# Kernel optimization log

Hardware: AMD Instinct MI355X
Metric: run time of the kernel (lower is better)

## Reference

```python
import jax, jax.numpy as jnp
import numpy as np

N_NODES = 50000
N_EDGES = 400000
IN_DIM = 64
HID = 128
HEADS = 4
NEG_SLOPE = 0.2


def gat_conv(x, src, dst, W, a_src, a_dst, b, heads, out_ch, concat):
    N = x.shape[0]
    h = (x @ W).reshape(N, heads, out_ch)                 # [N,H,C]
    alpha_s = jnp.einsum('nhc,hc->nh', h, a_src)          # [N,H]
    alpha_d = jnp.einsum('nhc,hc->nh', h, a_dst)
    e = jax.nn.leaky_relu(alpha_s[src] + alpha_d[dst], NEG_SLOPE)  # [E,H]
    m = jax.ops.segment_max(e, dst, num_segments=N)
    m = jnp.where(jnp.isfinite(m), m, 0.0)
    ex = jnp.exp(e - m[dst])
    s = jax.ops.segment_sum(ex, dst, num_segments=N)
    alpha = ex / s[dst]                                   # segment softmax over incoming edges
    out = jax.ops.segment_sum(h[src] * alpha[:, :, None], dst, num_segments=N)  # [N,H,C]
    out = out.reshape(N, heads * out_ch) if concat else out.mean(axis=1)
    return out + b


def setup_inputs() -> dict:
    key = jax.random.key(0)
    ks = jax.random.split(key, 20)
    g = lambda i, shape, sc: (jax.random.normal(ks[i], shape, jnp.float32) * sc)
    x = g(0, (N_NODES, IN_DIM), 1.0)
    edge_index = jax.random.randint(ks[1], (2, N_EDGES), 0, N_NODES, dtype=jnp.int32)
    d = {
        'x': x, 'edge_index': edge_index,
        'W1': g(2, (IN_DIM, HEADS * HID), 0.1), 'a_src1': g(3, (HEADS, HID), 0.1), 'a_dst1': g(4, (HEADS, HID), 0.1), 'b1': jnp.zeros((HEADS * HID,), jnp.float32),
        'W2': g(5, (HEADS * HID, HEADS * HID), 0.05), 'a_src2': g(6, (HEADS, HID), 0.1), 'a_dst2': g(7, (HEADS, HID), 0.1), 'b2': jnp.zeros((HEADS * HID,), jnp.float32),
        'W3': g(8, (HEADS * HID, HID), 0.05), 'a_src3': g(9, (1, HID), 0.1), 'a_dst3': g(10, (1, HID), 0.1), 'b3': jnp.zeros((HID,), jnp.float32),
        'fc1_w': g(11, (HID, HID // 2), 0.1), 'fc1_b': jnp.zeros((HID // 2,), jnp.float32),
        'fc2_w': g(12, (HID // 2, 1), 0.1), 'fc2_b': jnp.zeros((1,), jnp.float32),
    }
    return d


def reference(x, edge_index, W1, a_src1, a_dst1, b1, W2, a_src2, a_dst2, b2, W3, a_src3, a_dst3, b3, fc1_w, fc1_b, fc2_w, fc2_b):
    N = x.shape[0]
    loop = jnp.arange(N, dtype=edge_index.dtype)
    src = jnp.concatenate([edge_index[0], loop])  # PyG GATConv adds self-loops by default
    dst = jnp.concatenate([edge_index[1], loop])
    h = jax.nn.elu(gat_conv(x, src, dst, W1, a_src1, a_dst1, b1, HEADS, HID, True))
    h = jax.nn.elu(gat_conv(h, src, dst, W2, a_src2, a_dst2, b2, HEADS, HID, True))
    h = jax.nn.elu(gat_conv(h, src, dst, W3, a_src3, a_dst3, b3, 1, HID, False))
    h = jax.nn.relu(h @ fc1_w + fc1_b)
    return jax.nn.sigmoid(h @ fc2_w + fc2_b)  # [N, 1]
```

## Files before the change

kernel.cpp:

```cpp
#include <hip/hip_runtime.h>
#include <math.h>

typedef __attribute__((ext_vector_type(8))) short short8;
typedef __attribute__((ext_vector_type(4))) float f32x4;
typedef unsigned short u16;
typedef unsigned int u32;

__device__ inline u16 f2b(float f) {
  u32 u = __float_as_uint(f);
  return (u16)((u + 0x7FFFu + ((u >> 16) & 1u)) >> 16);
}
__device__ inline float b2f(u16 b) { return __uint_as_float((u32)b << 16); }
__device__ inline float lrelu(float v) { return v > 0.f ? v : 0.2f * v; }

__device__ inline void gld_lds16(const void* g, void* l) {
  __builtin_amdgcn_global_load_lds((const __attribute__((address_space(1))) void*)g,
                                   (__attribute__((address_space(3))) void*)l, 16, 0, 0);
}

__global__ void fused_prep(const float* __restrict__ x, u16* __restrict__ xb, int NX,
                           const float* __restrict__ W1, u16* __restrict__ Wt1,
                           const float* __restrict__ W2, u16* __restrict__ Wt2,
                           const float* __restrict__ W3, u16* __restrict__ Wt3,
                           const int* __restrict__ ei, int E0, int ET,
                           int* __restrict__ deg) {
  int i = blockIdx.x * blockDim.x + threadIdx.x;
  if (i < NX) {
    xb[i] = f2b(x[i]);
    return;
  }
  i -= NX;
  if (i < 64 * 512) {
    int k = i / 512, n = i % 512;
    Wt1[n * 64 + k] = f2b(W1[i]);
    return;
  }
  i -= 64 * 512;
  if (i < 512 * 512) {
    int k = i / 512, n = i % 512;
    Wt2[n * 512 + k] = f2b(W2[i]);
    return;
  }
  i -= 512 * 512;
  if (i < 512 * 128) {
    int k = i / 128, n = i % 128;
    Wt3[n * 512 + k] = f2b(W3[i]);
    return;
  }
  i -= 512 * 128;
  if (i < ET) {
    int d = (i < E0) ? ei[E0 + i] : (i - E0);
    atomicAdd(&deg[d], 1);
  }
}

__global__ __launch_bounds__(256) void gemm_bf16_gat(
    const u16* __restrict__ A, const u16* __restrict__ Bt, u16* __restrict__ Hb,
    const float* __restrict__ a_src, const float* __restrict__ a_dst,
    float* __restrict__ aS, float* __restrict__ aD, int M, int HC, int K, int Hh,
    int gy, int nStrips) {
  int mIdx, nIdx;
  if (nStrips == 4) {
    int l = blockIdx.x;
    int xcd = l & 7, k = l >> 3;
    nIdx = k & 3;
    mIdx = xcd + 8 * (k >> 2);
    if (mIdx >= gy) return;
  } else {
    mIdx = blockIdx.x;
    nIdx = 0;
  }
  __shared__ u16 As[128 * 32];
  __shared__ u16 Bs[128 * 32];
  __shared__ float sRed[2][2][128];
  const int tid = threadIdx.x;
  const int w = tid >> 6, lane = tid & 63;
  const int wm = w >> 1, wn = w & 1;
  const int q = lane >> 4, l15 = lane & 15;
  const int nBase = nIdx * 128;
  const int mBase = mIdx * 128;
  const int h = nBase >> 7;
  const int srow = lane >> 2;
  const int skc = (lane & 3) * 8;

  f32x4 acc[4][4];
#pragma unroll
  for (int i = 0; i < 4; ++i)
#pragma unroll
    for (int j = 0; j < 4; ++j) acc[i][j] = (f32x4){0.f, 0.f, 0.f, 0.f};

  for (int k0 = 0; k0 < K; k0 += 32) {
#pragma unroll
    for (int r = 0; r < 2; ++r) {
      int lrow = w * 32 + r * 16 + srow;
      int ga = mBase + lrow;
      if (ga >= M) ga = M - 1;
      gld_lds16(A + (size_t)ga * K + k0 + skc, &As[(w * 32 + r * 16) * 32]);
      int gb = nBase + lrow;
      gld_lds16(Bt + (size_t)gb * K + k0 + skc, &Bs[(w * 32 + r * 16) * 32]);
    }
    __syncthreads();
    short8 af[4], bf[4];
#pragma unroll
    for (int i = 0; i < 4; ++i)
      af[i] = *(const short8*)&As[(wm * 64 + i * 16 + l15) * 32 + q * 8];
#pragma unroll
    for (int j = 0; j < 4; ++j)
      bf[j] = *(const short8*)&Bs[(wn * 64 + j * 16 + l15) * 32 + q * 8];
#pragma unroll
    for (int i = 0; i < 4; ++i)
#pragma unroll
      for (int j = 0; j < 4; ++j)
        acc[i][j] = __builtin_amdgcn_mfma_f32_16x16x32_bf16(af[i], bf[j], acc[i][j], 0, 0, 0);
    __syncthreads();
  }

  float asv[4], adv[4];
#pragma unroll
  for (int j = 0; j < 4; ++j) {
    int cw = wn * 64 + j * 16 + l15;
    asv[j] = a_src[h * 128 + cw];
    adv[j] = a_dst[h * 128 + cw];
  }
#pragma unroll
  for (int mi = 0; mi < 4; ++mi) {
#pragma unroll
    for (int r = 0; r < 4; ++r) {
      int row = mBase + wm * 64 + mi * 16 + q * 4 + r;
      float s = 0.f, d = 0.f;
#pragma unroll
      for (int j = 0; j < 4; ++j) {
        float v = acc[mi][j][r];
        s = fmaf(v, asv[j], s);
        d = fmaf(v, adv[j], d);
        if (row < M) Hb[(size_t)row * HC + nBase + wn * 64 + j * 16 + l15] = f2b(v);
      }
#pragma unroll
      for (int o = 8; o; o >>= 1) {
        s += __shfl_xor(s, o);
        d += __shfl_xor(d, o);
      }
      if (l15 == 0) {
        int lr = wm * 64 + mi * 16 + q * 4 + r;
        sRed[0][wn][lr] = s;
        sRed[1][wn][lr] = d;
      }
    }
  }
  __syncthreads();
  if (tid < 128) {
    int row = mBase + tid;
    if (row < M) {
      aS[(size_t)row * Hh + h] = sRed[0][0][tid] + sRed[0][1][tid];
      aD[(size_t)row * Hh + h] = sRed[1][0][tid] + sRed[1][1][tid];
    }
  }
}

__global__ __launch_bounds__(256) void scan_chunk(const int* __restrict__ deg,
                                                  int* __restrict__ incl,
                                                  int* __restrict__ bsums, int N) {
  __shared__ int sdata[256];
  const int t = threadIdx.x;
  const int base = blockIdx.x * 2048;
  int v[8];
  int sum = 0;
#pragma unroll
  for (int i = 0; i < 8; ++i) {
    int idx = base + t * 8 + i;
    v[i] = (idx < N) ? deg[idx] : 0;
    sum += v[i];
  }
  sdata[t] = sum;
  __syncthreads();
  for (int off = 1; off < 256; off <<= 1) {
    int x = (t >= off) ? sdata[t - off] : 0;
    __syncthreads();
    sdata[t] += x;
    __syncthreads();
  }
  int run = (t > 0) ? sdata[t - 1] : 0;
#pragma unroll
  for (int i = 0; i < 8; ++i) {
    int idx = base + t * 8 + i;
    run += v[i];
    if (idx < N) incl[idx] = run;
  }
  if (t == 255) bsums[blockIdx.x] = sdata[255];
}

__global__ void scan_final(const int* __restrict__ incl, const int* __restrict__ bsums,
                           int* __restrict__ rowptr, int N, int nb) {
  int i = blockIdx.x * blockDim.x + threadIdx.x;
  if (i >= N) return;
  int chunk = i >> 11;
  int pre = 0;
  for (int j = 0; j < chunk; ++j) pre += bsums[j];
  rowptr[i + 1] = incl[i] + pre;
  if (i == 0) rowptr[0] = 0;
}

__global__ void csr_fill(const int* __restrict__ ei, int E0, int ET,
                         const int* __restrict__ rowptr, int* __restrict__ cnt,
                         int* __restrict__ csr_src) {
  int e = blockIdx.x * blockDim.x + threadIdx.x;
  if (e >= ET) return;
  int s, d;
  if (e < E0) { s = ei[e]; d = ei[E0 + e]; }
  else        { s = e - E0; d = e - E0; }
  int pos = atomicAdd(&cnt[d], 1);
  csr_src[rowptr[d] + pos] = s;
}

#define ACC8(pv, wgt)                                                  \
  acc[0] = fmaf(wgt, __uint_as_float(pv.x << 16), acc[0]);             \
  acc[1] = fmaf(wgt, __uint_as_float(pv.x & 0xffff0000u), acc[1]);     \
  acc[2] = fmaf(wgt, __uint_as_float(pv.y << 16), acc[2]);             \
  acc[3] = fmaf(wgt, __uint_as_float(pv.y & 0xffff0000u), acc[3]);     \
  acc[4] = fmaf(wgt, __uint_as_float(pv.z << 16), acc[4]);             \
  acc[5] = fmaf(wgt, __uint_as_float(pv.z & 0xffff0000u), acc[5]);     \
  acc[6] = fmaf(wgt, __uint_as_float(pv.w << 16), acc[6]);             \
  acc[7] = fmaf(wgt, __uint_as_float(pv.w & 0xffff0000u), acc[7]);

__global__ __launch_bounds__(256) void gat_fused_agg(
    const int* __restrict__ rowptr, const int* __restrict__ csr_src,
    const u16* __restrict__ Hb, const float* __restrict__ aSb,
    const float* __restrict__ aDb, const float* __restrict__ bias,
    u16* __restrict__ outB, float* __restrict__ outF, int N) {
  const int wid = (int)((blockIdx.x * (blockDim.x >> 6)) + (threadIdx.x >> 6));
  const int lane = threadIdx.x & 63;
  if (wid >= N) return;
  const int beg = rowptr[wid];
  const int deg = rowptr[wid + 1] - beg;

  const int h = lane >> 4;
  const int e16 = lane & 15;
  const int c0 = lane * 8;
  const int hbase = lane & 48;
  const float adh = aDb[(size_t)wid * 4 + h];
  float acc[8] = {};

  if (deg <= 16) {
    int srcv = 0;
    if (e16 < deg) srcv = csr_src[beg + e16];
    float av = aSb[(size_t)srcv * 4 + h];
    uint4 pC[4];
#pragma unroll
    for (int j = 0; j < 4; ++j)
      if (j < deg) {
        int s = __shfl(srcv, j);
        pC[j] = *(const uint4*)&Hb[(size_t)s * 512 + c0];
      }
    float l = (e16 < deg) ? lrelu(av + adh) : -1e30f;
    float m = l;
#pragma unroll
    for (int o = 8; o; o >>= 1) m = fmaxf(m, __shfl_xor(m, o));
    float pexp = (e16 < deg) ? __expf(l - m) : 0.f;
    float cs = pexp;
#pragma unroll
    for (int o = 8; o; o >>= 1) cs += __shfl_xor(cs, o);
    pexp *= (1.f / cs);
    int e = 0;
    for (; e + 4 < deg; e += 4) {
      uint4 pN[4];
      int rem = deg - e - 4;
#pragma unroll
      for (int j = 0; j < 4; ++j)
        if (j < rem) {
          int s = __shfl(srcv, e + 4 + j);
          pN[j] = *(const uint4*)&Hb[(size_t)s * 512 + c0];
        }
#pragma unroll
      for (int j = 0; j < 4; ++j) {
        float wgt = __shfl(pexp, hbase | (e + j));
        ACC8(pC[j], wgt)
      }
#pragma unroll
      for (int j = 0; j < 4; ++j) pC[j] = pN[j];
    }
#pragma unroll
    for (int j = 0; j < 4; ++j)
      if (j < deg - e) {
        float wgt = __shfl(pexp, hbase | (e + j));
        ACC8(pC[j], wgt)
      }
  } else {
    float m = -1e30f, ssum = 0.f;
    for (int c = 0; c < deg; c += 16) {
      const int ce = min(16, deg - c);
      int srcv = 0;
      float l = -1e30f;
      if (e16 < ce) {
        srcv = csr_src[beg + c + e16];
        l = lrelu(aSb[(size_t)srcv * 4 + h] + adh);
      }
      float cm = l;
#pragma unroll
      for (int o = 8; o; o >>= 1) cm = fmaxf(cm, __shfl_xor(cm, o));
      float pexp, cs;
      if (c == 0) {
        m = cm;
        pexp = __expf(l - m);
        cs = pexp;
#pragma unroll
        for (int o = 8; o; o >>= 1) cs += __shfl_xor(cs, o);
        ssum = cs;
      } else {
        float newm = fmaxf(m, cm);
        float r = __expf(m - newm);
        m = newm;
        pexp = __expf(l - m);
        cs = pexp;
#pragma unroll
        for (int o = 8; o; o >>= 1) cs += __shfl_xor(cs, o);
        ssum = ssum * r + cs;
#pragma unroll
        for (int i = 0; i < 8; ++i) acc[i] *= r;
      }
      int e = 0;
      for (; e + 4 <= ce; e += 4) {
        int se0 = __shfl(srcv, e + 0), se1 = __shfl(srcv, e + 1);
        int se2 = __shfl(srcv, e + 2), se3 = __shfl(srcv, e + 3);
        float w0 = __shfl(pexp, hbase | (e + 0)), w1 = __shfl(pexp, hbase | (e + 1));
        float w2 = __shfl(pexp, hbase | (e + 2)), w3 = __shfl(pexp, hbase | (e + 3));
        uint4 p0 = *(const uint4*)&Hb[(size_t)se0 * 512 + c0];
        uint4 p1 = *(const uint4*)&Hb[(size_t)se1 * 512 + c0];
        uint4 p2 = *(const uint4*)&Hb[(size_t)se2 * 512 + c0];
        uint4 p3 = *(const uint4*)&Hb[(size_t)se3 * 512 + c0];
        ACC8(p0, w0)
        ACC8(p1, w1)
        ACC8(p2, w2)
        ACC8(p3, w3)
      }
      for (; e < ce; ++e) {
        int se = __shfl(srcv, e);
        float wgt = __shfl(pexp, hbase | e);
        uint4 pv = *(const uint4*)&Hb[(size_t)se * 512 + c0];
        ACC8(pv, wgt)
      }
    }
    const float inv = 1.f / ssum;
#pragma unroll
    for (int i = 0; i < 8; ++i) acc[i] *= inv;
  }

  float bv[8];
  *(float4*)&bv[0] = *(const float4*)&bias[c0];
  *(float4*)&bv[4] = *(const float4*)&bias[c0 + 4];
  u16 packed[8];
#pragma unroll
  for (int i = 0; i < 8; ++i) {
    float v = acc[i] + bv[i];
    v = v > 0.f ? v : expm1f(v);
    acc[i] = v;
    packed[i] = f2b(v);
  }
  if (outB) *(uint4*)&outB[(size_t)wid * 512 + c0] = *(const uint4*)packed;
  if (outF) {
    *(float4*)&outF[(size_t)wid * 512 + c0] = make_float4(acc[0], acc[1], acc[2], acc[3]);
    *(float4*)&outF[(size_t)wid * 512 + c0 + 4] =
        make_float4(acc[4], acc[5], acc[6], acc[7]);
  }
}

__global__ __launch_bounds__(256) void gat_agg_h1(
    const int* __restrict__ rowptr, const int* __restrict__ csr_src,
    const u16* __restrict__ Hb, const float* __restrict__ aSb,
    const float* __restrict__ aDb, const float* __restrict__ bias,
    float* __restrict__ outF, int N) {
  const int wid = (int)((blockIdx.x * (blockDim.x >> 6)) + (threadIdx.x >> 6));
  const int lane = threadIdx.x & 63;
  if (wid >= N) return;
  const int beg = rowptr[wid];
  const int deg = rowptr[wid + 1] - beg;
  const int g = lane & 15;
  const int es = lane >> 4;
  const int c0 = g * 8;
  const float adh = aDb[wid];
  float acc[8] = {};

  if (deg <= 64) {
    int srcv = 0;
    if (lane < deg) srcv = csr_src[beg + lane];
    float av = aSb[srcv];
    const int dm1 = deg - 1;
    uint4 pC;
    {
      int s = __shfl(srcv, min(es, dm1));
      pC = *(const uint4*)&Hb[(size_t)s * 128 + c0];
    }
    float l = (lane < deg) ? lrelu(av + adh) : -1e30f;
    float m = l;
#pragma unroll
    for (int o = 32; o; o >>= 1) m = fmaxf(m, __shfl_xor(m, o));
    float pexp = (lane < deg) ? __expf(l - m) : 0.f;
    float cs = pexp;
#pragma unroll
    for (int o = 32; o; o >>= 1) cs += __shfl_xor(cs, o);
    pexp *= (1.f / cs);
    int t = 0;
    for (; t + 4 < deg; t += 4) {
      uint4 pN;
      {
        int s = __shfl(srcv, min(t + 4 + es, dm1));
        pN = *(const uint4*)&Hb[(size_t)s * 128 + c0];
      }
      float w = __shfl(pexp, t + es);
      ACC8(pC, w)
      pC = pN;
    }
    {
      int idx = t + es;
      float w = __shfl(pexp, min(idx, dm1));
      if (idx > dm1) w = 0.f;
      ACC8(pC, w)
    }
  } else {
    float m = -1e30f, ssum = 0.f;
    for (int c = 0; c < deg; c += 64) {
      const int ce = min(64, deg - c);
      int srcv = 0;
      float l = -1e30f;
      if (lane < ce) {
        srcv = csr_src[beg + c + lane];
        l = lrelu(aSb[srcv] + adh);
      }
      float cm = l;
#pragma unroll
      for (int o = 32; o; o >>= 1) cm = fmaxf(cm, __shfl_xor(cm, o));
      float pexp, cs;
      if (c == 0) {
        m = cm;
        pexp = __expf(l - m);
        cs = pexp;
#pragma unroll
        for (int o = 32; o; o >>= 1) cs += __shfl_xor(cs, o);
        ssum = cs;
      } else {
        float newm = fmaxf(m, cm);
        float r = __expf(m - newm);
        m = newm;
        pexp = __expf(l - m);
        cs = pexp;
#pragma unroll
        for (int o = 32; o; o >>= 1) cs += __shfl_xor(cs, o);
        ssum = ssum * r + cs;
#pragma unroll
        for (int i = 0; i < 8; ++i) acc[i] *= r;
      }
      for (int t = 0; t < ce; t += 4) {
        int idx = t + es;
        int se = __shfl(srcv, idx & 63);
        float wgt = __shfl(pexp, idx & 63);
        if (idx < ce) {
          uint4 pv = *(const uint4*)&Hb[(size_t)se * 128 + c0];
          ACC8(pv, wgt)
        }
      }
    }
    const float inv = 1.f / ssum;
#pragma unroll
    for (int i = 0; i < 8; ++i) acc[i] *= inv;
  }
#pragma unroll
  for (int i = 0; i < 8; ++i) {
    acc[i] += __shfl_xor(acc[i], 16);
    acc[i] += __shfl_xor(acc[i], 32);
  }
  if (lane < 16) {
    float o[8];
#pragma unroll
    for (int i = 0; i < 8; ++i) {
      float v = acc[i] + bias[c0 + i];
      o[i] = v > 0.f ? v : expm1f(v);
    }
    *(float4*)&outF[(size_t)wid * 128 + c0] = make_float4(o[0], o[1], o[2], o[3]);
    *(float4*)&outF[(size_t)wid * 128 + c0 + 4] = make_float4(o[4], o[5], o[6], o[7]);
  }
}

__global__ __launch_bounds__(256) void fc_head(const float* __restrict__ A,
                                               const float* __restrict__ B,
                                               const float* __restrict__ bias,
                                               const float* __restrict__ w2,
                                               const float* __restrict__ b2,
                                               float* __restrict__ out, int M) {
  __shared__ float As[16][64];
  __shared__ float Bs[16][64];
  __shared__ float sP[64][17];
  const int tid = threadIdx.x;
  const int tx = tid & 15, ty = tid >> 4;
  const int mBase = blockIdx.y * 64;
  const int aRow = tid >> 2;
  const int aK = (tid & 3) << 2;
  const int bC = tid & 63;
  const int bR0 = tid >> 6;
  const int K = 128, N = 64;
  float acc[4][4] = {};
  for (int k0 = 0; k0 < K; k0 += 16) {
    float4 av = make_float4(0.f, 0.f, 0.f, 0.f);
    int gr = mBase + aRow;
    if (gr < M) av = *(const float4*)&A[(size_t)gr * K + k0 + aK];
    As[aK + 0][aRow] = av.x;
    As[aK + 1][aRow] = av.y;
    As[aK + 2][aRow] = av.z;
    As[aK + 3][aRow] = av.w;
#pragma unroll
    for (int i = 0; i < 4; ++i) {
      int r = bR0 + i * 4;
      Bs[r][bC] = B[(size_t)(k0 + r) * N + bC];
    }
    __syncthreads();
#pragma unroll
    for (int k = 0; k < 16; ++k) {
      float4 a = *(const float4*)&As[k][ty * 4];
      float4 b = *(const float4*)&Bs[k][tx * 4];
      float ar[4] = {a.x, a.y, a.z, a.w};
      float br[4] = {b.x, b.y, b.z, b.w};
#pragma unroll
      for (int i = 0; i < 4; ++i)
#pragma unroll
        for (int j = 0; j < 4; ++j) acc[i][j] = fmaf(ar[i], br[j], acc[i][j]);
    }
    __syncthreads();
  }
  float4 bv = *(const float4*)&bias[tx * 4];
  float4 wv = *(const float4*)&w2[tx * 4];
#pragma unroll
  for (int i = 0; i < 4; ++i) {
    float p = 0.f;
    p = fmaf(fmaxf(acc[i][0] + bv.x, 0.f), wv.x, p);
    p = fmaf(fmaxf(acc[i][1] + bv.y, 0.f), wv.y, p);
    p = fmaf(fmaxf(acc[i][2] + bv.z, 0.f), wv.z, p);
    p = fmaf(fmaxf(acc[i][3] + bv.w, 0.f), wv.w, p);
    sP[ty * 4 + i][tx] = p;
  }
  __syncthreads();
  if (tid < 64) {
    int row = mBase + tid;
    if (row < M) {
      float s = 0.f;
#pragma unroll
      for (int t = 0; t < 16; ++t) s += sP[tid][t];
      out[row] = 1.f / (1.f + expf(-(s + b2[0])));
    }
  }
}

extern "C" void kernel_launch(void* const* d_in, const int* in_sizes, int n_in,
                              void* d_out, int out_size, void* d_ws, size_t ws_size,
                              hipStream_t stream) {
  const float* x    = (const float*)d_in[0];
  const int*   ei   = (const int*)d_in[1];
  const float* W1   = (const float*)d_in[2];
  const float* as1  = (const float*)d_in[3];
  const float* ad1  = (const float*)d_in[4];
  const float* b1   = (const float*)d_in[5];
  const float* W2   = (const float*)d_in[6];
  const float* as2  = (const float*)d_in[7];
  const float* ad2  = (const float*)d_in[8];
  const float* b2   = (const float*)d_in[9];
  const float* W3   = (const float*)d_in[10];
  const float* as3  = (const float*)d_in[11];
  const float* ad3  = (const float*)d_in[12];
  const float* b3   = (const float*)d_in[13];
  const float* fc1w = (const float*)d_in[14];
  const float* fc1b = (const float*)d_in[15];
  const float* fc2w = (const float*)d_in[16];
  const float* fc2b = (const float*)d_in[17];
  float* out = (float*)d_out;

  const int N  = in_sizes[0] / 64;
  const int E0 = in_sizes[1] / 2;
  const int ET = E0 + N;

  char* ws = (char*)d_ws;
  size_t off = 0;
  auto alloc = [&](size_t bytes) -> void* {
    void* p = ws + off;
    off += (bytes + 255) & ~(size_t)255;
    return p;
  };
  u16*   bufXb   = (u16*)alloc((size_t)N * 512 * 2);
  u16*   bufHb   = (u16*)alloc((size_t)N * 512 * 2);
  float* bufF    = (float*)alloc((size_t)N * 128 * 4);
  float* aS      = (float*)alloc((size_t)N * 4 * 4);
  float* aD      = (float*)alloc((size_t)N * 4 * 4);
  u16*   Wt1     = (u16*)alloc((size_t)512 * 64 * 2);
  u16*   Wt2     = (u16*)alloc((size_t)512 * 512 * 2);
  u16*   Wt3     = (u16*)alloc((size_t)128 * 512 * 2);
  int*   degcnt  = (int*)alloc((size_t)2 * N * 4);
  int*   deg     = degcnt;
  int*   cnt     = degcnt + N;
  int*   incl    = (int*)alloc((size_t)N * 4);
  int*   rowptr  = (int*)alloc((size_t)(N + 1) * 4);
  int*   bsums   = (int*)alloc(256 * 4);
  int*   csr_src = (int*)alloc((size_t)ET * 4);
  (void)ws_size; (void)n_in; (void)out_size;

  hipMemsetAsync(degcnt, 0, (size_t)2 * N * 4, stream);
  const int NX = N * 64;
  const int prepTotal = NX + 64 * 512 + 512 * 512 + 512 * 128 + ET;
  hipLaunchKernelGGL(fused_prep, dim3((prepTotal + 255) / 256), dim3(256), 0, stream, x,
                     bufXb, NX, W1, Wt1, W2, Wt2, W3, Wt3, ei, E0, ET, deg);

  int nb = (N + 2047) / 2048;
  hipLaunchKernelGGL(scan_chunk, dim3(nb), dim3(256), 0, stream, deg, incl, bsums, N);
  hipLaunchKernelGGL(scan_final, dim3((N + 255) / 256), dim3(256), 0, stream, incl, bsums,
                     rowptr, N, nb);
  int eb = (ET + 255) / 256;
  hipLaunchKernelGGL(csr_fill, dim3(eb), dim3(256), 0, stream, ei, E0, ET, rowptr, cnt,
                     csr_src);

  const int gy = (N + 127) / 128;
  const int grid4 = ((gy + 7) / 8) * 8 * 4;

  hipLaunchKernelGGL(gemm_bf16_gat, dim3(grid4), dim3(256), 0, stream, bufXb, Wt1, bufHb,
                     as1, ad1, aS, aD, N, 512, 64, 4, gy, 4);
  hipLaunchKernelGGL(gat_fused_agg, dim3((N + 3) / 4), dim3(256), 0, stream, rowptr,
                     csr_src, bufHb, aS, aD, b1, bufXb, nullptr, N);
  hipLaunchKernelGGL(gemm_bf16_gat, dim3(grid4), dim3(256), 0, stream, bufXb, Wt2, bufHb,
                     as2, ad2, aS, aD, N, 512, 512, 4, gy, 4);
  hipLaunchKernelGGL(gat_fused_agg, dim3((N + 3) / 4), dim3(256), 0, stream, rowptr,
                     csr_src, bufHb, aS, aD, b2, bufXb, nullptr, N);
  hipLaunchKernelGGL(gemm_bf16_gat, dim3(gy), dim3(256), 0, stream, bufXb, Wt3, bufHb,
                     as3, ad3, aS, aD, N, 128, 512, 1, gy, 1);
  hipLaunchKernelGGL(gat_agg_h1, dim3((N + 3) / 4), dim3(256), 0, stream, rowptr, csr_src,
                     bufHb, aS, aD, b3, bufF, N);

  hipLaunchKernelGGL(fc_head, dim3(1, (N + 63) / 64), dim3(256), 0, stream, bufF, fc1w,
                     fc1b, fc2w, fc2b, out, N);
}
```

Before: 451.5 us.

## Process two destination nodes per wavefront in GAT aggregation kernels

Each wavefront in both aggregation kernels now handles two consecutive destination nodes. It interleaves their index loads, softmax reductions and gather prefetches, which is meant to raise memory-level parallelism and hide gather latency. The grid is halved to match, and the exact expm1f in ELU is replaced with a fast __expf-based version. This costs more registers per thread, so occupancy may fall, and nodes with very different degrees in the same wavefront are now serialized.

```diff
diff --git a/kernel.cpp b/kernel.cpp
--- a/kernel.cpp
+++ b/kernel.cpp
@@ -12,6 +12,7 @@
 }
 __device__ inline float b2f(u16 b) { return __uint_as_float((u32)b << 16); }
 __device__ inline float lrelu(float v) { return v > 0.f ? v : 0.2f * v; }
+__device__ inline float elu1(float v) { return v > 0.f ? v : __expf(v) - 1.f; }
 
 __device__ inline void gld_lds16(const void* g, void* l) {
   __builtin_amdgcn_global_load_lds((const __attribute__((address_space(1))) void*)g,
@@ -212,34 +213,21 @@
   csr_src[rowptr[d] + pos] = s;
 }
 
-#define ACC8(pv, wgt)                                                  \
-  acc[0] = fmaf(wgt, __uint_as_float(pv.x << 16), acc[0]);             \
-  acc[1] = fmaf(wgt, __uint_as_float(pv.x & 0xffff0000u), acc[1]);     \
-  acc[2] = fmaf(wgt, __uint_as_float(pv.y << 16), acc[2]);             \
-  acc[3] = fmaf(wgt, __uint_as_float(pv.y & 0xffff0000u), acc[3]);     \
-  acc[4] = fmaf(wgt, __uint_as_float(pv.z << 16), acc[4]);             \
-  acc[5] = fmaf(wgt, __uint_as_float(pv.z & 0xffff0000u), acc[5]);     \
-  acc[6] = fmaf(wgt, __uint_as_float(pv.w << 16), acc[6]);             \
-  acc[7] = fmaf(wgt, __uint_as_float(pv.w & 0xffff0000u), acc[7]);
-
-__global__ __launch_bounds__(256) void gat_fused_agg(
-    const int* __restrict__ rowptr, const int* __restrict__ csr_src,
-    const u16* __restrict__ Hb, const float* __restrict__ aSb,
-    const float* __restrict__ aDb, const float* __restrict__ bias,
-    u16* __restrict__ outB, float* __restrict__ outF, int N) {
-  const int wid = (int)((blockIdx.x * (blockDim.x >> 6)) + (threadIdx.x >> 6));
-  const int lane = threadIdx.x & 63;
-  if (wid >= N) return;
-  const int beg = rowptr[wid];
-  const int deg = rowptr[wid + 1] - beg;
-
-  const int h = lane >> 4;
-  const int e16 = lane & 15;
-  const int c0 = lane * 8;
-  const int hbase = lane & 48;
-  const float adh = aDb[(size_t)wid * 4 + h];
-  float acc[8] = {};
-
+#define ACC8(A, pv, wgt)                                             \
+  A[0] = fmaf(wgt, __uint_as_float(pv.x << 16), A[0]);               \
+  A[1] = fmaf(wgt, __uint_as_float(pv.x & 0xffff0000u), A[1]);       \
+  A[2] = fmaf(wgt, __uint_as_float(pv.y << 16), A[2]);               \
+  A[3] = fmaf(wgt, __uint_as_float(pv.y & 0xffff0000u), A[3]);       \
+  A[4] = fmaf(wgt, __uint_as_float(pv.z << 16), A[4]);               \
+  A[5] = fmaf(wgt, __uint_as_float(pv.z & 0xffff0000u), A[5]);       \
+  A[6] = fmaf(wgt, __uint_as_float(pv.w << 16), A[6]);               \
+  A[7] = fmaf(wgt, __uint_as_float(pv.w & 0xffff0000u), A[7]);
+
+__device__ inline void agg4_node(const int* __restrict__ csr_src,
+                                 const u16* __restrict__ Hb,
+                                 const float* __restrict__ aSb, float adh, int beg,
+                                 int deg, int e16, int h, int c0, int hbase,
+                                 float* acc) {
   if (deg <= 16) {
     int srcv = 0;
     if (e16 < deg) srcv = csr_src[beg + e16];
@@ -273,7 +261,7 @@
 #pragma unroll
       for (int j = 0; j < 4; ++j) {
         float wgt = __shfl(pexp, hbase | (e + j));
-        ACC8(pC[j], wgt)
+        ACC8(acc, pC[j], wgt)
       }
 #pragma unroll
       for (int j = 0; j < 4; ++j) pC[j] = pN[j];
@@ -282,7 +270,7 @@
     for (int j = 0; j < 4; ++j)
       if (j < deg - e) {
         float wgt = __shfl(pexp, hbase | (e + j));
-        ACC8(pC[j], wgt)
+        ACC8(acc, pC[j], wgt)
       }
   } else {
     float m = -1e30f, ssum = 0.f;
@@ -327,58 +315,176 @@
         uint4 p1 = *(const uint4*)&Hb[(size_t)se1 * 512 + c0];
         uint4 p2 = *(const uint4*)&Hb[(size_t)se2 * 512 + c0];
         uint4 p3 = *(const uint4*)&Hb[(size_t)se3 * 512 + c0];
-        ACC8(p0, w0)
-        ACC8(p1, w1)
-        ACC8(p2, w2)
-        ACC8(p3, w3)
+        ACC8(acc, p0, w0)
+        ACC8(acc, p1, w1)
+        ACC8(acc, p2, w2)
+        ACC8(acc, p3, w3)
       }
       for (; e < ce; ++e) {
         int se = __shfl(srcv, e);
         float wgt = __shfl(pexp, hbase | e);
         uint4 pv = *(const uint4*)&Hb[(size_t)se * 512 + c0];
-        ACC8(pv, wgt)
+        ACC8(acc, pv, wgt)
       }
     }
     const float inv = 1.f / ssum;
 #pragma unroll
     for (int i = 0; i < 8; ++i) acc[i] *= inv;
+  }
+}
+
+__global__ __launch_bounds__(256) void gat_fused_agg(
+    const int* __restrict__ rowptr, const int* __restrict__ csr_src,
+    const u16* __restrict__ Hb, const float* __restrict__ aSb,
+    const float* __restrict__ aDb, const float* __restrict__ bias,
+    u16* __restrict__ outB, float* __restrict__ outF, int N) {
+  const int wv = (int)((blockIdx.x * (blockDim.x >> 6)) + (threadIdx.x >> 6));
+  const int wid0 = wv * 2, wid1 = wid0 + 1;
+  const int lane = threadIdx.x & 63;
+  if (wid0 >= N) return;
+  const bool has1 = (wid1 < N);
+
+  const int h = lane >> 4;
+  const int e16 = lane & 15;
+  const int c0 = lane * 8;
+  const int hbase = lane & 48;
+
+  const int beg0 = rowptr[wid0];
+  const int mid  = rowptr[wid1];
+  const int end1 = has1 ? rowptr[wid1 + 1] : mid;
+  const int deg0 = mid - beg0;
+  const int beg1 = mid;
+  const int deg1 = end1 - mid;
+  const float adh0 = aDb[(size_t)wid0 * 4 + h];
+  const float adh1 = has1 ? aDb[(size_t)wid1 * 4 + h] : 0.f;
+
+  float acc0[8] = {}, acc1[8] = {};
+
+  if (deg0 <= 16 && deg1 <= 16) {
+    int s0 = 0, s1 = 0;
+    if (e16 < deg0) s0 = csr_src[beg0 + e16];
+    if (e16 < deg1) s1 = csr_src[beg1 + e16];
+    float av0 = aSb[(size_t)s0 * 4 + h];
+    float av1 = aSb[(size_t)s1 * 4 + h];
+    uint4 pA[4], pB[4];
+#pragma unroll
+    for (int j = 0; j < 4; ++j)
+      if (j < deg0) {
+        int s = __shfl(s0, j);
+        pA[j] = *(const uint4*)&Hb[(size_t)s * 512 + c0];
+      }
+#pragma unroll
+    for (int j = 0; j < 4; ++j)
+      if (j < deg1) {
+        int s = __shfl(s1, j);
+        pB[j] = *(const uint4*)&Hb[(size_t)s * 512 + c0];
+      }
+    float l0 = (e16 < deg0) ? lrelu(av0 + adh0) : -1e30f;
+    float l1 = (e16 < deg1) ? lrelu(av1 + adh1) : -1e30f;
+    float m0 = l0, m1 = l1;
+#pragma unroll
+    for (int o = 8; o; o >>= 1) {
+      m0 = fmaxf(m0, __shfl_xor(m0, o));
+      m1 = fmaxf(m1, __shfl_xor(m1, o));
+    }
+    float p0 = (e16 < deg0) ? __expf(l0 - m0) : 0.f;
+    float p1 = (e16 < deg1) ? __expf(l1 - m1) : 0.f;
+    float cs0 = p0, cs1 = p1;
+#pragma unroll
+    for (int o = 8; o; o >>= 1) {
+      cs0 += __shfl_xor(cs0, o);
+      cs1 += __shfl_xor(cs1, o);
+    }
+    p0 *= (1.f / cs0);
+    p1 *= (1.f / cs1);
+    int e = 0;
+    for (; e + 4 < deg0; e += 4) {
+      uint4 pN[4];
+      int rem = deg0 - e - 4;
+#pragma unroll
+      for (int j = 0; j < 4; ++j)
+        if (j < rem) {
+          int s = __shfl(s0, e + 4 + j);
+          pN[j] = *(const uint4*)&Hb[(size_t)s * 512 + c0];
+        }
+#pragma unroll
+      for (int j = 0; j < 4; ++j) {
+        float wgt = __shfl(p0, hbase | (e + j));
+        ACC8(acc0, pA[j], wgt)
+      }
+#pragma unroll
+      for (int j = 0; j < 4; ++j) pA[j] = pN[j];
+    }
+#pragma unroll
+    for (int j = 0; j < 4; ++j)
+      if (j < deg0 - e) {
+        float wgt = __shfl(p0, hbase | (e + j));
+        ACC8(acc0, pA[j], wgt)
+      }
+    e = 0;
+    for (; e + 4 < deg1; e += 4) {
+      uint4 pN[4];
+      int rem = deg1 - e - 4;
+#pragma unroll
+      for (int j = 0; j < 4; ++j)
+        if (j < rem) {
+          int s = __shfl(s1, e + 4 + j);
+          pN[j] = *(const uint4*)&Hb[(size_t)s * 512 + c0];
+        }
+#pragma unroll
+      for (int j = 0; j < 4; ++j) {
+        float wgt = __shfl(p1, hbase | (e + j));
+        ACC8(acc1, pB[j], wgt)
+      }
+#pragma unroll
+      for (int j = 0; j < 4; ++j) pB[j] = pN[j];
+    }
+#pragma unroll
+    for (int j = 0; j < 4; ++j)
+      if (j < deg1 - e) {
+        float wgt = __shfl(p1, hbase | (e + j));
+        ACC8(acc1, pB[j], wgt)
+      }
+  } else {
+    agg4_node(csr_src, Hb, aSb, adh0, beg0, deg0, e16, h, c0, hbase, acc0);
+    if (has1) agg4_node(csr_src, Hb, aSb, adh1, beg1, deg1, e16, h, c0, hbase, acc1);
   }
 
   float bv[8];
   *(float4*)&bv[0] = *(const float4*)&bias[c0];
   *(float4*)&bv[4] = *(const float4*)&bias[c0 + 4];
-  u16 packed[8];
+  u16 pk0[8], pk1[8];
 #pragma unroll
   for (int i = 0; i < 8; ++i) {
-    float v = acc[i] + bv[i];
-    v = v > 0.f ? v : expm1f(v);
-    acc[i] = v;
-    packed[i] = f2b(v);
-  }
-  if (outB) *(uint4*)&outB[(size_t)wid * 512 + c0] = *(const uint4*)packed;
+    float v0 = elu1(acc0[i] + bv[i]);
+    acc0[i] = v0;
+    pk0[i] = f2b(v0);
+    float v1 = elu1(acc1[i] + bv[i]);
+    acc1[i] = v1;
+    pk1[i] = f2b(v1);
+  }
+  if (outB) {
+    *(uint4*)&outB[(size_t)wid0 * 512 + c0] = *(const uint4*)pk0;
+    if (has1) *(uint4*)&outB[(size_t)wid1 * 512 + c0] = *(const uint4*)pk1;
+  }
   if (outF) {
-    *(float4*)&outF[(size_t)wid * 512 + c0] = make_float4(acc[0], acc[1], acc[2], acc[3]);
-    *(float4*)&outF[(size_t)wid * 512 + c0 + 4] =
-        make_float4(acc[4], acc[5], acc[6], acc[7]);
-  }
-}
-
-__global__ __launch_bounds__(256) void gat_agg_h1(
-    const int* __restrict__ rowptr, const int* __restrict__ csr_src,
-    const u16* __restrict__ Hb, const float* __restrict__ aSb,
-    const float* __restrict__ aDb, const float* __restrict__ bias,
-    float* __restrict__ outF, int N) {
-  const int wid = (int)((blockIdx.x * (blockDim.x >> 6)) + (threadIdx.x >> 6));
-  const int lane = threadIdx.x & 63;
-  if (wid >= N) return;
-  const int beg = rowptr[wid];
-  const int deg = rowptr[wid + 1] - beg;
-  const int g = lane & 15;
-  const int es = lane >> 4;
-  const int c0 = g * 8;
-  const float adh = aDb[wid];
-  float acc[8] = {};
-
+    *(float4*)&outF[(size_t)wid0 * 512 + c0] =
+        make_float4(acc0[0], acc0[1], acc0[2], acc0[3]);
+    *(float4*)&outF[(size_t)wid0 * 512 + c0 + 4] =
+        make_float4(acc0[4], acc0[5], acc0[6], acc0[7]);
+    if (has1) {
+      *(float4*)&outF[(size_t)wid1 * 512 + c0] =
+          make_float4(acc1[0], acc1[1], acc1[2], acc1[3]);
+      *(float4*)&outF[(size_t)wid1 * 512 + c0 + 4] =
+          make_float4(acc1[4], acc1[5], acc1[6], acc1[7]);
+    }
+  }
+}
+
+__device__ inline void agg1_node(const int* __restrict__ csr_src,
+                                 const u16* __restrict__ Hb,
+                                 const float* __restrict__ aSb, float adh, int beg,
+                                 int deg, int lane, int es, int c0, float* acc) {
   if (deg <= 64) {
     int srcv = 0;
     if (lane < deg) srcv = csr_src[beg + lane];
@@ -406,14 +512,14 @@
         pN = *(const uint4*)&Hb[(size_t)s * 128 + c0];
       }
       float w = __shfl(pexp, t + es);
-      ACC8(pC, w)
+      ACC8(acc, pC, w)
       pC = pN;
     }
     {
       int idx = t + es;
       float w = __shfl(pexp, min(idx, dm1));
       if (idx > dm1) w = 0.f;
-      ACC8(pC, w)
+      ACC8(acc, pC, w)
     }
   } else {
     float m = -1e30f, ssum = 0.f;
@@ -454,7 +560,7 @@
         float wgt = __shfl(pexp, idx & 63);
         if (idx < ce) {
           uint4 pv = *(const uint4*)&Hb[(size_t)se * 128 + c0];
-          ACC8(pv, wgt)
+          ACC8(acc, pv, wgt)
         }
       }
     }
@@ -462,20 +568,130 @@
 #pragma unroll
     for (int i = 0; i < 8; ++i) acc[i] *= inv;
   }
+}
+
+__global__ __launch_bounds__(256) void gat_agg_h1(
+    const int* __restrict__ rowptr, const int* __restrict__ csr_src,
+    const u16* __restrict__ Hb, const float* __restrict__ aSb,
+    const float* __restrict__ aDb, const float* __restrict__ bias,
+    float* __restrict__ outF, int N) {
+  const int wv = (int)((blockIdx.x * (blockDim.x >> 6)) + (threadIdx.x >> 6));
+  const int wid0 = wv * 2, wid1 = wid0 + 1;
+  const int lane = threadIdx.x & 63;
+  if (wid0 >= N) return;
+  const bool has1 = (wid1 < N);
+  const int g = lane & 15;
+  const int es = lane >> 4;
+  const int c0 = g * 8;
+
+  const int beg0 = rowptr[wid0];
+  const int mid  = rowptr[wid1];
+  const int end1 = has1 ? rowptr[wid1 + 1] : mid;
+  const int deg0 = mid - beg0;
+  const int beg1 = mid;
+  const int deg1 = end1 - mid;
+  const float adh0 = aDb[wid0];
+  const float adh1 = has1 ? aDb[wid1] : 0.f;
+  float acc0[8] = {}, acc1[8] = {};
+
+  if (deg0 <= 64 && deg1 <= 64) {
+    int s0 = 0, s1 = 0;
+    if (lane < deg0) s0 = csr_src[beg0 + lane];
+    if (lane < deg1) s1 = csr_src[beg1 + lane];
+    float av0 = aSb[s0];
+    float av1 = aSb[s1];
+    const int dm10 = deg0 - 1, dm11 = deg1 - 1;
+    uint4 pA, pB;
+    {
+      int s = __shfl(s0, min(es, dm10));
+      pA = *(const uint4*)&Hb[(size_t)s * 128 + c0];
+    }
+    if (has1) {
+      int s = __shfl(s1, min(es, max(dm11, 0)));
+      pB = *(const uint4*)&Hb[(size_t)s * 128 + c0];
+    }
+    float l0 = (lane < deg0) ? lrelu(av0 + adh0) : -1e30f;
+    float l1 = (lane < deg1) ? lrelu(av1 + adh1) : -1e30f;
+    float m0 = l0, m1 = l1;
+#pragma unroll
+    for (int o = 32; o; o >>= 1) {
+      m0 = fmaxf(m0, __shfl_xor(m0, o));
+      m1 = fmaxf(m1, __shfl_xor(m1, o));
+    }
+    float p0 = (lane < deg0) ? __expf(l0 - m0) : 0.f;
+    float p1 = (lane < deg1) ? __expf(l1 - m1) : 0.f;
+    float cs0 = p0, cs1 = p1;
+#pragma unroll
+    for (int o = 32; o; o >>= 1) {
+      cs0 += __shfl_xor(cs0, o);
+      cs1 += __shfl_xor(cs1, o);
+    }
+    p0 *= (1.f / cs0);
+    p1 *= (1.f / cs1);
+    int t = 0;
+    for (; t + 4 < deg0; t += 4) {
+      uint4 pN;
+      {
+        int s = __shfl(s0, min(t + 4 + es, dm10));
+        pN = *(const uint4*)&Hb[(size_t)s * 128 + c0];
+      }
+      float w = __shfl(p0, t + es);
+      ACC8(acc0, pA, w)
+      pA = pN;
+    }
+    {
+      int idx = t + es;
+      float w = __shfl(p0, min(idx, dm10));
+      if (idx > dm10) w = 0.f;
+      ACC8(acc0, pA, w)
+    }
+    if (has1) {
+      t = 0;
+      for (; t + 4 < deg1; t += 4) {
+        uint4 pN;
+        {
+          int s = __shfl(s1, min(t + 4 + es, dm11));
+          pN = *(const uint4*)&Hb[(size_t)s * 128 + c0];
+        }
+        float w = __shfl(p1, t + es);
+        ACC8(acc1, pB, w)
+        pB = pN;
+      }
+      {
+        int idx = t + es;
+        float w = __shfl(p1, min(idx, dm11));
+        if (idx > dm11) w = 0.f;
+        ACC8(acc1, pB, w)
+      }
+    }
+  } else {
+    agg1_node(csr_src, Hb, aSb, adh0, beg0, deg0, lane, es, c0, acc0);
+    if (has1) agg1_node(csr_src, Hb, aSb, adh1, beg1, deg1, lane, es, c0, acc1);
+  }
+
 #pragma unroll
   for (int i = 0; i < 8; ++i) {
-    acc[i] += __shfl_xor(acc[i], 16);
-    acc[i] += __shfl_xor(acc[i], 32);
+    acc0[i] += __shfl_xor(acc0[i], 16);
+    acc0[i] += __shfl_xor(acc0[i], 32);
+    acc1[i] += __shfl_xor(acc1[i], 16);
+    acc1[i] += __shfl_xor(acc1[i], 32);
   }
   if (lane < 16) {
-    float o[8];
+    float o0[8], o1[8];
 #pragma unroll
     for (int i = 0; i < 8; ++i) {
-      float v = acc[i] + bias[c0 + i];
-      o[i] = v > 0.f ? v : expm1f(v);
-    }
-    *(float4*)&outF[(size_t)wid * 128 + c0] = make_float4(o[0], o[1], o[2], o[3]);
-    *(float4*)&outF[(size_t)wid * 128 + c0 + 4] = make_float4(o[4], o[5], o[6], o[7]);
+      float b = bias[c0 + i];
+      o0[i] = elu1(acc0[i] + b);
+      o1[i] = elu1(acc1[i] + b);
+    }
+    *(float4*)&outF[(size_t)wid0 * 128 + c0] = make_float4(o0[0], o0[1], o0[2], o0[3]);
+    *(float4*)&outF[(size_t)wid0 * 128 + c0 + 4] =
+        make_float4(o0[4], o0[5], o0[6], o0[7]);
+    if (has1) {
+      *(float4*)&outF[(size_t)wid1 * 128 + c0] = make_float4(o1[0], o1[1], o1[2], o1[3]);
+      *(float4*)&outF[(size_t)wid1 * 128 + c0 + 4] =
+          make_float4(o1[4], o1[5], o1[6], o1[7]);
+    }
   }
 }
 
@@ -614,18 +830,19 @@
 
   const int gy = (N + 127) / 128;
   const int grid4 = ((gy + 7) / 8) * 8 * 4;
+  const int aggGrid = (N + 7) / 8;
 
   hipLaunchKernelGGL(gemm_bf16_gat, dim3(grid4), dim3(256), 0, stream, bufXb, Wt1, bufHb,
                      as1, ad1, aS, aD, N, 512, 64, 4, gy, 4);
-  hipLaunchKernelGGL(gat_fused_agg, dim3((N + 3) / 4), dim3(256), 0, stream, rowptr,
+  hipLaunchKernelGGL(gat_fused_agg, dim3(aggGrid), dim3(256), 0, stream, rowptr,
                      csr_src, bufHb, aS, aD, b1, bufXb, nullptr, N);
   hipLaunchKernelGGL(gemm_bf16_gat, dim3(grid4), dim3(256), 0, stream, bufXb, Wt2, bufHb,
                      as2, ad2, aS, aD, N, 512, 512, 4, gy, 4);
-  hipLaunchKernelGGL(gat_fused_agg, dim3((N + 3) / 4), dim3(256), 0, stream, rowptr,
+  hipLaunchKernelGGL(gat_fused_agg, dim3(aggGrid), dim3(256), 0, stream, rowptr,
                      csr_src, bufHb, aS, aD, b2, bufXb, nullptr, N);
   hipLaunchKernelGGL(gemm_bf16_gat, dim3(gy), dim3(256), 0, stream, bufXb, Wt3, bufHb,
                      as3, ad3, aS, aD, N, 128, 512, 1, gy, 1);
-  hipLaunchKernelGGL(gat_agg_h1, dim3((N + 3) / 4), dim3(256), 0, stream, rowptr, csr_src,
+  hipLaunchKernelGGL(gat_agg_h1, dim3(aggGrid), dim3(256), 0, stream, rowptr, csr_src,
                      bufHb, aS, aD, b3, bufF, N);
 
   hipLaunchKernelGGL(fc_head, dim3(1, (N + 63) / 64), dim3(256), 0, stream, bufF, fc1w,
```

Measured after the change: 441.5 us. -2.2%, faster.

## Precompute per-edge attention logits in a separate kernel before aggregation

Applied to the files above, without the earlier changes.

Adds an edge_logits kernel that computes the leaky-ReLU of aS[src]+aD[dst] for every CSR edge and writes them to a buffer, with csr_fill now also recording each edge's destination. The aggregation kernels then read the precomputed logit instead of gathering aS by source index inside the serial softmax prologue. The goal is to take the dependent random gather off the aggregation critical path. In exchange it adds three kernel launches and extra global traffic for the logit and destination arrays. ELU's expm1f is also replaced with __expf(v)-1, which is cheaper but slightly less accurate near zero.

```diff
diff --git a/kernel.cpp b/kernel.cpp
--- a/kernel.cpp
+++ b/kernel.cpp
@@ -12,6 +12,7 @@
 }
 __device__ inline float b2f(u16 b) { return __uint_as_float((u32)b << 16); }
 __device__ inline float lrelu(float v) { return v > 0.f ? v : 0.2f * v; }
+__device__ inline float elu1(float v) { return v > 0.f ? v : __expf(v) - 1.f; }
 
 __device__ inline void gld_lds16(const void* g, void* l) {
   __builtin_amdgcn_global_load_lds((const __attribute__((address_space(1))) void*)g,
@@ -202,7 +203,7 @@
 
 __global__ void csr_fill(const int* __restrict__ ei, int E0, int ET,
                          const int* __restrict__ rowptr, int* __restrict__ cnt,
-                         int* __restrict__ csr_src) {
+                         int* __restrict__ csr_src, int* __restrict__ csr_dst) {
   int e = blockIdx.x * blockDim.x + threadIdx.x;
   if (e >= ET) return;
   int s, d;
@@ -210,23 +211,47 @@
   else        { s = e - E0; d = e - E0; }
   int pos = atomicAdd(&cnt[d], 1);
   csr_src[rowptr[d] + pos] = s;
-}
-
-#define ACC8(pv, wgt)                                                  \
-  acc[0] = fmaf(wgt, __uint_as_float(pv.x << 16), acc[0]);             \
-  acc[1] = fmaf(wgt, __uint_as_float(pv.x & 0xffff0000u), acc[1]);     \
-  acc[2] = fmaf(wgt, __uint_as_float(pv.y << 16), acc[2]);             \
-  acc[3] = fmaf(wgt, __uint_as_float(pv.y & 0xffff0000u), acc[3]);     \
-  acc[4] = fmaf(wgt, __uint_as_float(pv.z << 16), acc[4]);             \
-  acc[5] = fmaf(wgt, __uint_as_float(pv.z & 0xffff0000u), acc[5]);     \
-  acc[6] = fmaf(wgt, __uint_as_float(pv.w << 16), acc[6]);             \
-  acc[7] = fmaf(wgt, __uint_as_float(pv.w & 0xffff0000u), acc[7]);
+  csr_dst[rowptr[d] + pos] = d;
+}
+
+__global__ __launch_bounds__(256) void edge_logits(const int* __restrict__ csr_src,
+                                                   const int* __restrict__ csr_dst,
+                                                   const float* __restrict__ aS,
+                                                   const float* __restrict__ aD,
+                                                   float* __restrict__ elog, int ET,
+                                                   int Hh) {
+  int e = blockIdx.x * blockDim.x + threadIdx.x;
+  if (e >= ET) return;
+  int s = csr_src[e], d = csr_dst[e];
+  if (Hh == 4) {
+    float4 a = *(const float4*)&aS[(size_t)s * 4];
+    float4 b = *(const float4*)&aD[(size_t)d * 4];
+    float4 r;
+    r.x = lrelu(a.x + b.x);
+    r.y = lrelu(a.y + b.y);
+    r.z = lrelu(a.z + b.z);
+    r.w = lrelu(a.w + b.w);
+    *(float4*)&elog[(size_t)e * 4] = r;
+  } else {
+    elog[e] = lrelu(aS[s] + aD[d]);
+  }
+}
+
+#define ACC8(A, pv, wgt)                                             \
+  A[0] = fmaf(wgt, __uint_as_float(pv.x << 16), A[0]);               \
+  A[1] = fmaf(wgt, __uint_as_float(pv.x & 0xffff0000u), A[1]);       \
+  A[2] = fmaf(wgt, __uint_as_float(pv.y << 16), A[2]);               \
+  A[3] = fmaf(wgt, __uint_as_float(pv.y & 0xffff0000u), A[3]);       \
+  A[4] = fmaf(wgt, __uint_as_float(pv.z << 16), A[4]);               \
+  A[5] = fmaf(wgt, __uint_as_float(pv.z & 0xffff0000u), A[5]);       \
+  A[6] = fmaf(wgt, __uint_as_float(pv.w << 16), A[6]);               \
+  A[7] = fmaf(wgt, __uint_as_float(pv.w & 0xffff0000u), A[7]);
 
 __global__ __launch_bounds__(256) void gat_fused_agg(
     const int* __restrict__ rowptr, const int* __restrict__ csr_src,
-    const u16* __restrict__ Hb, const float* __restrict__ aSb,
-    const float* __restrict__ aDb, const float* __restrict__ bias,
-    u16* __restrict__ outB, float* __restrict__ outF, int N) {
+    const u16* __restrict__ Hb, const float* __restrict__ elog,
+    const float* __restrict__ bias, u16* __restrict__ outB,
+    float* __restrict__ outF, int N) {
   const int wid = (int)((blockIdx.x * (blockDim.x >> 6)) + (threadIdx.x >> 6));
   const int lane = threadIdx.x & 63;
   if (wid >= N) return;
@@ -237,13 +262,15 @@
   const int e16 = lane & 15;
   const int c0 = lane * 8;
   const int hbase = lane & 48;
-  const float adh = aDb[(size_t)wid * 4 + h];
   float acc[8] = {};
 
   if (deg <= 16) {
     int srcv = 0;
-    if (e16 < deg) srcv = csr_src[beg + e16];
-    float av = aSb[(size_t)srcv * 4 + h];
+    float l = -1e30f;
+    if (e16 < deg) {
+      srcv = csr_src[beg + e16];
+      l = elog[(size_t)(beg + e16) * 4 + h];
+    }
     uint4 pC[4];
 #pragma unroll
     for (int j = 0; j < 4; ++j)
@@ -251,7 +278,6 @@
         int s = __shfl(srcv, j);
         pC[j] = *(const uint4*)&Hb[(size_t)s * 512 + c0];
       }
-    float l = (e16 < deg) ? lrelu(av + adh) : -1e30f;
     float m = l;
 #pragma unroll
     for (int o = 8; o; o >>= 1) m = fmaxf(m, __shfl_xor(m, o));
@@ -273,7 +299,7 @@
 #pragma unroll
       for (int j = 0; j < 4; ++j) {
         float wgt = __shfl(pexp, hbase | (e + j));
-        ACC8(pC[j], wgt)
+        ACC8(acc, pC[j], wgt)
       }
 #pragma unroll
       for (int j = 0; j < 4; ++j) pC[j] = pN[j];
@@ -282,7 +308,7 @@
     for (int j = 0; j < 4; ++j)
       if (j < deg - e) {
         float wgt = __shfl(pexp, hbase | (e + j));
-        ACC8(pC[j], wgt)
+        ACC8(acc, pC[j], wgt)
       }
   } else {
     float m = -1e30f, ssum = 0.f;
@@ -292,7 +318,7 @@
       float l = -1e30f;
       if (e16 < ce) {
         srcv = csr_src[beg + c + e16];
-        l = lrelu(aSb[(size_t)srcv * 4 + h] + adh);
+        l = elog[(size_t)(beg + c + e16) * 4 + h];
       }
       float cm = l;
 #pragma unroll
@@ -327,16 +353,16 @@
         uint4 p1 = *(const uint4*)&Hb[(size_t)se1 * 512 + c0];
         uint4 p2 = *(const uint4*)&Hb[(size_t)se2 * 512 + c0];
         uint4 p3 = *(const uint4*)&Hb[(size_t)se3 * 512 + c0];
-        ACC8(p0, w0)
-        ACC8(p1, w1)
-        ACC8(p2, w2)
-        ACC8(p3, w3)
+        ACC8(acc, p0, w0)
+        ACC8(acc, p1, w1)
+        ACC8(acc, p2, w2)
+        ACC8(acc, p3, w3)
       }
       for (; e < ce; ++e) {
         int se = __shfl(srcv, e);
         float wgt = __shfl(pexp, hbase | e);
         uint4 pv = *(const uint4*)&Hb[(size_t)se * 512 + c0];
-        ACC8(pv, wgt)
+        ACC8(acc, pv, wgt)
       }
     }
     const float inv = 1.f / ssum;
@@ -350,8 +376,7 @@
   u16 packed[8];
 #pragma unroll
   for (int i = 0; i < 8; ++i) {
-    float v = acc[i] + bv[i];
-    v = v > 0.f ? v : expm1f(v);
+    float v = elu1(acc[i] + bv[i]);
     acc[i] = v;
     packed[i] = f2b(v);
   }
@@ -365,9 +390,8 @@
 
 __global__ __launch_bounds__(256) void gat_agg_h1(
     const int* __restrict__ rowptr, const int* __restrict__ csr_src,
-    const u16* __restrict__ Hb, const float* __restrict__ aSb,
-    const float* __restrict__ aDb, const float* __restrict__ bias,
-    float* __restrict__ outF, int N) {
+    const u16* __restrict__ Hb, const float* __restrict__ elog,
+    const float* __restrict__ bias, float* __restrict__ outF, int N) {
   const int wid = (int)((blockIdx.x * (blockDim.x >> 6)) + (threadIdx.x >> 6));
   const int lane = threadIdx.x & 63;
   if (wid >= N) return;
@@ -376,20 +400,21 @@
   const int g = lane & 15;
   const int es = lane >> 4;
   const int c0 = g * 8;
-  const float adh = aDb[wid];
   float acc[8] = {};
 
   if (deg <= 64) {
     int srcv = 0;
-    if (lane < deg) srcv = csr_src[beg + lane];
-    float av = aSb[srcv];
+    float l = -1e30f;
+    if (lane < deg) {
+      srcv = csr_src[beg + lane];
+      l = elog[beg + lane];
+    }
     const int dm1 = deg - 1;
     uint4 pC;
     {
       int s = __shfl(srcv, min(es, dm1));
       pC = *(const uint4*)&Hb[(size_t)s * 128 + c0];
     }
-    float l = (lane < deg) ? lrelu(av + adh) : -1e30f;
     float m = l;
 #pragma unroll
     for (int o = 32; o; o >>= 1) m = fmaxf(m, __shfl_xor(m, o));
@@ -406,14 +431,14 @@
         pN = *(const uint4*)&Hb[(size_t)s * 128 + c0];
       }
       float w = __shfl(pexp, t + es);
-      ACC8(pC, w)
+      ACC8(acc, pC, w)
       pC = pN;
     }
     {
       int idx = t + es;
       float w = __shfl(pexp, min(idx, dm1));
       if (idx > dm1) w = 0.f;
-      ACC8(pC, w)
+      ACC8(acc, pC, w)
     }
   } else {
     float m = -1e30f, ssum = 0.f;
@@ -423,7 +448,7 @@
       float l = -1e30f;
       if (lane < ce) {
         srcv = csr_src[beg + c + lane];
-        l = lrelu(aSb[srcv] + adh);
+        l = elog[beg + c + lane];
       }
       float cm = l;
 #pragma unroll
@@ -454,7 +479,7 @@
         float wgt = __shfl(pexp, idx & 63);
         if (idx < ce) {
           uint4 pv = *(const uint4*)&Hb[(size_t)se * 128 + c0];
-          ACC8(pv, wgt)
+          ACC8(acc, pv, wgt)
         }
       }
     }
@@ -470,10 +495,7 @@
   if (lane < 16) {
     float o[8];
 #pragma unroll
-    for (int i = 0; i < 8; ++i) {
-      float v = acc[i] + bias[c0 + i];
-      o[i] = v > 0.f ? v : expm1f(v);
-    }
+    for (int i = 0; i < 8; ++i) o[i] = elu1(acc[i] + bias[c0 + i]);
     *(float4*)&outF[(size_t)wid * 128 + c0] = make_float4(o[0], o[1], o[2], o[3]);
     *(float4*)&outF[(size_t)wid * 128 + c0 + 4] = make_float4(o[4], o[5], o[6], o[7]);
   }
@@ -596,6 +618,8 @@
   int*   rowptr  = (int*)alloc((size_t)(N + 1) * 4);
   int*   bsums   = (int*)alloc(256 * 4);
   int*   csr_src = (int*)alloc((size_t)ET * 4);
+  int*   csr_dst = (int*)alloc((size_t)ET * 4);
+  float* elog    = (float*)alloc((size_t)ET * 4 * 4);
   (void)ws_size; (void)n_in; (void)out_size;
 
   hipMemsetAsync(degcnt, 0, (size_t)2 * N * 4, stream);
@@ -610,23 +634,30 @@
                      rowptr, N, nb);
   int eb = (ET + 255) / 256;
   hipLaunchKernelGGL(csr_fill, dim3(eb), dim3(256), 0, stream, ei, E0, ET, rowptr, cnt,
-                     csr_src);
+                     csr_src, csr_dst);
 
   const int gy = (N + 127) / 128;
   const int grid4 = ((gy + 7) / 8) * 8 * 4;
+  const int aggGrid = (N + 3) / 4;
 
   hipLaunchKernelGGL(gemm_bf16_gat, dim3(grid4), dim3(256), 0, stream, bufXb, Wt1, bufHb,
                      as1, ad1, aS, aD, N, 512, 64, 4, gy, 4);
-  hipLaunchKernelGGL(gat_fused_agg, dim3((N + 3) / 4), dim3(256), 0, stream, rowptr,
-                     csr_src, bufHb, aS, aD, b1, bufXb, nullptr, N);
+  hipLaunchKernelGGL(edge_logits, dim3(eb), dim3(256), 0, stream, csr_src, csr_dst, aS,
+                     aD, elog, ET, 4);
+  hipLaunchKernelGGL(gat_fused_agg, dim3(aggGrid), dim3(256), 0, stream, rowptr,
+                     csr_src, bufHb, elog, b1, bufXb, nullptr, N);
   hipLaunchKernelGGL(gemm_bf16_gat, dim3(grid4), dim3(256), 0, stream, bufXb, Wt2, bufHb,
                      as2, ad2, aS, aD, N, 512, 512, 4, gy, 4);
-  hipLaunchKernelGGL(gat_fused_agg, dim3((N + 3) / 4), dim3(256), 0, stream, rowptr,
-                     csr_src, bufHb, aS, aD, b2, bufXb, nullptr, N);
+  hipLaunchKernelGGL(edge_logits, dim3(eb), dim3(256), 0, stream, csr_src, csr_dst, aS,
+                     aD, elog, ET, 4);
+  hipLaunchKernelGGL(gat_fused_agg, dim3(aggGrid), dim3(256), 0, stream, rowptr,
+                     csr_src, bufHb, elog, b2, bufXb, nullptr, N);
   hipLaunchKernelGGL(gemm_bf16_gat, dim3(gy), dim3(256), 0, stream, bufXb, Wt3, bufHb,
                      as3, ad3, aS, aD, N, 128, 512, 1, gy, 1);
-  hipLaunchKernelGGL(gat_agg_h1, dim3((N + 3) / 4), dim3(256), 0, stream, rowptr, csr_src,
-                     bufHb, aS, aD, b3, bufF, N);
+  hipLaunchKernelGGL(edge_logits, dim3(eb), dim3(256), 0, stream, csr_src, csr_dst, aS,
+                     aD, elog, ET, 1);
+  hipLaunchKernelGGL(gat_agg_h1, dim3(aggGrid), dim3(256), 0, stream, rowptr, csr_src,
+                     bufHb, elog, b3, bufF, N);
 
   hipLaunchKernelGGL(fc_head, dim3(1, (N + 63) / 64), dim3(256), 0, stream, bufF, fc1w,
                      fc1b, fc2w, fc2b, out, N);
```

Result: no change. 452.2 us (+0.1%).
